# Performance work log

Measured on AMD Instinct MI355X. Metric: run time of the kernel, lower is better.

## Reference

```python
import jax, jax.numpy as jnp
import numpy as np

FP8_MAX = 448.0  # max finite value of float8_e4m3fn
F8 = jnp.float8_e4m3fn


def setup_inputs() -> dict:
    key = jax.random.key(0)
    kx, kw, kb = jax.random.split(key, 3)
    B, S, K, N = 4, 2048, 4096, 16384
    x = jax.random.normal(kx, (B, S, K), dtype=jnp.float32)
    # Pre-quantized symmetric per-tensor FP8 weight: simulate quantization of a
    # realistically initialized fp32 weight with scale ws.
    ws = jnp.float32(0.01)
    w_fp32 = jax.random.normal(kw, (N, K), dtype=jnp.float32) * 0.02
    weight = jnp.clip(w_fp32 / ws, -FP8_MAX, FP8_MAX).astype(F8)  # [N, K] fp8
    weight_scale = jnp.full((1,), ws, dtype=jnp.float32)  # per-tensor strategy
    bias = jax.random.normal(kb, (N,), dtype=jnp.float32) * 0.01
    return {"x": x, "weight": weight, "weight_scale": weight_scale, "bias": bias}


def reference(x, weight, weight_scale, bias):
    # Dynamic per-tensor fp8 quantization of the activation (torchao
    # _input_activation_quant_func_fp8 with PerTensor granularity):
    # (input_scale * weight_scale), plus bias.
    amax = jnp.max(jnp.abs(x))
    x_scale = jnp.maximum(amax, jnp.float32(1e-12)) / FP8_MAX
    xq = jnp.clip(x / x_scale, -FP8_MAX, FP8_MAX).astype(F8).astype(jnp.float32)
    w = weight.astype(jnp.float32)  # [N, K]
    out = jnp.einsum("bsk,nk->bsn", xq, w)  # [B, S, N]
    out = out * (x_scale * weight_scale[0]) + bias
    return out
```

## Files before the change

### kernel.cpp

```cpp
#include <hip/hip_runtime.h>
#include <hip/hip_fp8.h>
#include <hip/hip_fp16.h>
#include <stdint.h>

#define FP8_MAX_V 448.0f

typedef float f32x16 __attribute__((ext_vector_type(16)));
typedef int i32x4 __attribute__((ext_vector_type(4)));
typedef int i32x8 __attribute__((ext_vector_type(8)));

__device__ __forceinline__ uint8_t cvt_fp8(float v) {
    return __hip_cvt_float_to_fp8(fminf(fmaxf(v, -FP8_MAX_V), FP8_MAX_V),
                                  __HIP_SATFINITE, __HIP_E4M3);
}

__global__ void fp8lin_probe(const uint32_t* __restrict__ w, unsigned* __restrict__ flag,
                             unsigned* __restrict__ amax_bits) {
    __shared__ unsigned s32, s16, s4;
    if (threadIdx.x == 0) { s32 = 0u; s16 = 0u; s4 = 0u; *amax_bits = 0u; }
    __syncthreads();
    unsigned o32 = 0u, o16 = 0u, o4 = 0u;
    for (int i = threadIdx.x; i < 4096; i += 256) {
        uint32_t v = w[i];
        o32 |= v & 0x000FFFFFu;
        uint32_t h0 = v & 0xFFFFu, h1 = v >> 16;
        o16 |= (h0 & 0x7Fu) | (h1 & 0x7Fu);
        o4  |= (h0 & 0x0Fu) | (h1 & 0x0Fu);
    }
    atomicOr(&s32, o32); atomicOr(&s16, o16); atomicOr(&s4, o4);
    __syncthreads();
    if (threadIdx.x == 0)
        *flag = (s32 == 0u) ? 0u : (s16 == 0u) ? 1u : (s4 == 0u) ? 2u : 3u;
}

__global__ void fp8lin_amax(const float4* __restrict__ x, unsigned* __restrict__ amax_bits, long n4) {
    float m = 0.f;
    long stride = (long)gridDim.x * blockDim.x;
    for (long i = blockIdx.x * (long)blockDim.x + threadIdx.x; i < n4; i += stride) {
        float4 v = x[i];
        m = fmaxf(m, fmaxf(fmaxf(fabsf(v.x), fabsf(v.y)), fmaxf(fabsf(v.z), fabsf(v.w))));
    }
#pragma unroll
    for (int o = 32; o; o >>= 1) m = fmaxf(m, __shfl_xor(m, o));
    if ((threadIdx.x & 63) == 0) atomicMax(amax_bits, __float_as_uint(m));
}

__global__ void fp8lin_quantpack(const float* __restrict__ x, const unsigned* __restrict__ amax_bits,
                                 uchar4* __restrict__ apack, int M, int K) {
    float s = fmaxf(__uint_as_float(*amax_bits), 1e-12f) / FP8_MAX_V;
    const int NKT = K >> 6;
    const long units = ((long)M * K) >> 2;
    long stride = (long)gridDim.x * blockDim.x;
    for (long u = blockIdx.x * (long)blockDim.x + threadIdx.x; u < units; u += stride) {
        long b2 = u & 7;
        long r = (u >> 3) & 31;
        long q = (u >> 8) & 1;
        long v = u >> 9;
        long row = (v / NKT) * 32 + r;
        long k = (v % NKT) * 64 + q * 32 + b2 * 4;
        float4 t = *(const float4*)(x + row * (long)K + k);
        uchar4 o;
        o.x = cvt_fp8(t.x / s); o.y = cvt_fp8(t.y / s);
        o.z = cvt_fp8(t.z / s); o.w = cvt_fp8(t.w / s);
        apack[u] = o;
    }
}

__global__ void fp8lin_packw(const void* __restrict__ wsrc, const unsigned* __restrict__ flag,
                             uint8_t* __restrict__ pack, int N, int K) {
    const int NKT = K >> 6;
    const long units = ((long)N * K) >> 6;
    unsigned f = *flag;
    long stride = (long)gridDim.x * blockDim.x;
    for (long u = blockIdx.x * (long)blockDim.x + threadIdx.x; u < units; u += stride) {
        int r = (int)(u & 31);
        long v = u >> 5;
        long row = (v / NKT) * 32 + r;
        long kbase = (long)(v % NKT) * 64;
        uint32_t wv[16];
        if (f == 0u) {
            const float4* s = (const float4*)((const float*)wsrc + row * K + kbase);
#pragma unroll
            for (int i = 0; i < 16; ++i) {
                float4 t = s[i];
                wv[i] = (uint32_t)cvt_fp8(t.x) | ((uint32_t)cvt_fp8(t.y) << 8) |
                        ((uint32_t)cvt_fp8(t.z) << 16) | ((uint32_t)cvt_fp8(t.w) << 24);
            }
        } else if (f == 1u) {
            const __half* s = (const __half*)wsrc + row * K + kbase;
#pragma unroll
            for (int i = 0; i < 16; ++i) {
                uint32_t a = 0;
#pragma unroll
                for (int j = 0; j < 4; ++j) a |= (uint32_t)cvt_fp8(__half2float(s[4 * i + j])) << (8 * j);
                wv[i] = a;
            }
        } else if (f == 2u) {
            const uint16_t* s = (const uint16_t*)wsrc + row * K + kbase;
#pragma unroll
            for (int i = 0; i < 16; ++i) {
                uint32_t a = 0;
#pragma unroll
                for (int j = 0; j < 4; ++j)
                    a |= (uint32_t)cvt_fp8(__uint_as_float((uint32_t)s[4 * i + j] << 16)) << (8 * j);
                wv[i] = a;
            }
        } else {
            const uint32_t* s = (const uint32_t*)((const uint8_t*)wsrc + row * K + kbase);
#pragma unroll
            for (int i = 0; i < 16; ++i) wv[i] = s[i];
        }
        uint8_t* d0 = pack + (v * 64 + r) * 32;
        uint8_t* d1 = pack + (v * 64 + 32 + r) * 32;
        i32x4 lo0 = { (int)wv[0], (int)wv[1], (int)wv[2], (int)wv[3] };
        i32x4 lo1 = { (int)wv[4], (int)wv[5], (int)wv[6], (int)wv[7] };
        i32x4 hi0 = { (int)wv[8], (int)wv[9], (int)wv[10], (int)wv[11] };
        i32x4 hi1 = { (int)wv[12], (int)wv[13], (int)wv[14], (int)wv[15] };
        *(i32x4*)(d0) = lo0; *(i32x4*)(d0 + 16) = lo1;
        *(i32x4*)(d1) = hi0; *(i32x4*)(d1 + 16) = hi1;
    }
}

#define BM 256
#define BN 128
#define BK 64

#define LOADF(bv, src, koff) do {                                      \
    const uint8_t* _p = (src) + (koff);                                \
    i32x4 _l0 = *(const i32x4*)(_p);                                   \
    i32x4 _l1 = *(const i32x4*)(_p + 16);                              \
    bv[0] = _l0[0]; bv[1] = _l0[1]; bv[2] = _l0[2]; bv[3] = _l0[3];    \
    bv[4] = _l1[0]; bv[5] = _l1[1]; bv[6] = _l1[2]; bv[7] = _l1[3];    \
} while (0)

#define MFMA_MX(A, B, C) __builtin_amdgcn_mfma_scale_f32_32x32x64_f8f6f4( \
    (A), (B), (C), 0, 0, 0, (int)0x7f7f7f7f, 0, (int)0x7f7f7f7f)

__global__ __launch_bounds__(256, 2) void fp8lin_gemm(
    const uint8_t* __restrict__ Apack,
    const uint8_t* __restrict__ Bpack,
    const unsigned* __restrict__ amax_bits,
    const float* __restrict__ wscale,
    const float* __restrict__ bias,
    float* __restrict__ out,
    int M, int N, int K) {
    const int tid = threadIdx.x;
    const int wid = tid >> 6;
    const int lane = tid & 63;
    const int wm = wid >> 1;
    const int wn = wid & 1;

    const int nbx = gridDim.x;
    const int orig = blockIdx.y * nbx + blockIdx.x;
    const int cpx = (gridDim.x * gridDim.y) >> 3;
    const int swzb = (orig & 7) * cpx + (orig >> 3);
    const int brow = (swzb / nbx) * BM;
    const int bcol = (swzb % nbx) * BN;

    const int NKT = K >> 6;
    const int mt0 = (brow >> 5) + wm * 4;
    const uint8_t* pA0 = Apack + ((size_t)(mt0 + 0) * NKT * 64 + lane) * 32;
    const uint8_t* pA1 = Apack + ((size_t)(mt0 + 1) * NKT * 64 + lane) * 32;
    const uint8_t* pA2 = Apack + ((size_t)(mt0 + 2) * NKT * 64 + lane) * 32;
    const uint8_t* pA3 = Apack + ((size_t)(mt0 + 3) * NKT * 64 + lane) * 32;
    const uint8_t* pB0 = Bpack + ((size_t)((bcol >> 5) + wn * 2) * NKT * 64 + lane) * 32;
    const uint8_t* pB1 = pB0 + (size_t)NKT * 2048;

    f32x16 acc[4][2];
#pragma unroll
    for (int mi = 0; mi < 4; ++mi)
#pragma unroll
        for (int ni = 0; ni < 2; ++ni)
#pragma unroll
            for (int r = 0; r < 16; ++r) acc[mi][ni][r] = 0.0f;

    i32x8 a0, a1, a2, a3, b0, b1;
    LOADF(a0, pA0, 0); LOADF(a1, pA1, 0);
    LOADF(a2, pA2, 0); LOADF(a3, pA3, 0);
    LOADF(b0, pB0, 0); LOADF(b1, pB1, 0);

    const int NT = K / BK;
#pragma unroll 1
    for (int t = 0; t < NT; ++t) {
        __builtin_amdgcn_s_setprio(1);
        acc[0][0] = MFMA_MX(a0, b0, acc[0][0]);
        acc[1][0] = MFMA_MX(a1, b0, acc[1][0]);
        acc[2][0] = MFMA_MX(a2, b0, acc[2][0]);
        acc[3][0] = MFMA_MX(a3, b0, acc[3][0]);
        acc[0][1] = MFMA_MX(a0, b1, acc[0][1]);
        acc[1][1] = MFMA_MX(a1, b1, acc[1][1]);
        acc[2][1] = MFMA_MX(a2, b1, acc[2][1]);
        acc[3][1] = MFMA_MX(a3, b1, acc[3][1]);
        __builtin_amdgcn_s_setprio(0);
        if (t + 1 < NT) {
            size_t off = (size_t)(t + 1) * 2048;
            LOADF(a0, pA0, off); LOADF(a1, pA1, off);
            LOADF(a2, pA2, off); LOADF(a3, pA3, off);
            LOADF(b0, pB0, off); LOADF(b1, pB1, off);
        }
    }

    float s = (fmaxf(__uint_as_float(*amax_bits), 1e-12f) / FP8_MAX_V) * wscale[0];
    const int l31 = lane & 31;
    const int q = lane >> 5;
    const int colg = bcol + wn * 64 + l31;
    const int rowg0 = brow + wm * 128 + 4 * q;
#pragma unroll
    for (int ni = 0; ni < 2; ++ni) {
        int col = colg + ni * 32;
        float bv = bias[col];
#pragma unroll
        for (int mi = 0; mi < 4; ++mi) {
            int rb = rowg0 + mi * 32;
#pragma unroll
            for (int reg = 0; reg < 16; ++reg) {
                int row = rb + (reg & 3) + 8 * (reg >> 2);
                __builtin_nontemporal_store(acc[mi][ni][reg] * s + bv,
                                            out + (size_t)row * N + col);
            }
        }
    }
}

extern "C" void kernel_launch(void* const* d_in, const int* in_sizes, int n_in,
                              void* d_out, int out_size, void* d_ws, size_t ws_size,
                              hipStream_t stream) {
    const float* x = (const float*)d_in[0];
    const void* w = d_in[1];
    const float* wscale = (const float*)d_in[2];
    const float* bias = (const float*)d_in[3];
    float* out = (float*)d_out;

    const int Bb = 4, S = 2048, K = 4096, N = 16384;
    const int M = Bb * S;
    const long nx = (long)M * K;

    unsigned* amax_bits = (unsigned*)d_ws;
    unsigned* wflag = (unsigned*)((char*)d_ws + 32);
    uint8_t* apack = (uint8_t*)((char*)d_ws + 256);
    uint8_t* bpack = (uint8_t*)((char*)d_ws + 256 + nx);

    fp8lin_probe<<<1, 256, 0, stream>>>((const uint32_t*)w, wflag, amax_bits);
    fp8lin_amax<<<2048, 256, 0, stream>>>((const float4*)x, amax_bits, nx / 4);
    fp8lin_quantpack<<<2048, 256, 0, stream>>>(x, amax_bits, (uchar4*)apack, M, K);
    fp8lin_packw<<<2048, 256, 0, stream>>>(w, wflag, bpack, N, K);

    dim3 grid(N / BN, M / BM);
    fp8lin_gemm<<<grid, 256, 0, stream>>>(apack, bpack, amax_bits, wscale, bias, out, M, N, K);
}
```

Baseline: 820.6 us.

## Software-pipeline GEMM loads with split MFMA halves and manual vmcnt waits

```diff
diff --git a/kernel.cpp b/kernel.cpp
--- a/kernel.cpp
+++ b/kernel.cpp
@@ -125,16 +125,33 @@
 #define BN 128
 #define BK 64
 
-#define LOADF(bv, src, koff) do {                                      \
-    const uint8_t* _p = (src) + (koff);                                \
+#define LDU(bv, ub, t) do {                                            \
+    const uint8_t* _p = (ub) + (size_t)(t) * 2048 + voff;              \
     i32x4 _l0 = *(const i32x4*)(_p);                                   \
     i32x4 _l1 = *(const i32x4*)(_p + 16);                              \
     bv[0] = _l0[0]; bv[1] = _l0[1]; bv[2] = _l0[2]; bv[3] = _l0[3];    \
     bv[4] = _l1[0]; bv[5] = _l1[1]; bv[6] = _l1[2]; bv[7] = _l1[3];    \
 } while (0)
 
+#define WAITVM(N) asm volatile("s_waitcnt vmcnt(" #N ")" ::: "memory")
+
 #define MFMA_MX(A, B, C) __builtin_amdgcn_mfma_scale_f32_32x32x64_f8f6f4( \
     (A), (B), (C), 0, 0, 0, (int)0x7f7f7f7f, 0, (int)0x7f7f7f7f)
+
+#define P1(B0, B1) do {                               \
+    __builtin_amdgcn_s_setprio(1);                    \
+    acc[0][0] = MFMA_MX(a0, B0, acc[0][0]);           \
+    acc[1][0] = MFMA_MX(a1, B0, acc[1][0]);           \
+    acc[0][1] = MFMA_MX(a0, B1, acc[0][1]);           \
+    acc[1][1] = MFMA_MX(a1, B1, acc[1][1]);           \
+    __builtin_amdgcn_s_setprio(0); } while (0)
+#define P2(B0, B1) do {                               \
+    __builtin_amdgcn_s_setprio(1);                    \
+    acc[2][0] = MFMA_MX(a2, B0, acc[2][0]);           \
+    acc[3][0] = MFMA_MX(a3, B0, acc[3][0]);           \
+    acc[2][1] = MFMA_MX(a2, B1, acc[2][1]);           \
+    acc[3][1] = MFMA_MX(a3, B1, acc[3][1]);           \
+    __builtin_amdgcn_s_setprio(0); } while (0)
 
 __global__ __launch_bounds__(256, 2) void fp8lin_gemm(
     const uint8_t* __restrict__ Apack,
@@ -158,13 +175,15 @@
     const int bcol = (swzb % nbx) * BN;
 
     const int NKT = K >> 6;
+    const size_t TSTRIDE = (size_t)NKT * 2048;
     const int mt0 = (brow >> 5) + wm * 4;
-    const uint8_t* pA0 = Apack + ((size_t)(mt0 + 0) * NKT * 64 + lane) * 32;
-    const uint8_t* pA1 = Apack + ((size_t)(mt0 + 1) * NKT * 64 + lane) * 32;
-    const uint8_t* pA2 = Apack + ((size_t)(mt0 + 2) * NKT * 64 + lane) * 32;
-    const uint8_t* pA3 = Apack + ((size_t)(mt0 + 3) * NKT * 64 + lane) * 32;
-    const uint8_t* pB0 = Bpack + ((size_t)((bcol >> 5) + wn * 2) * NKT * 64 + lane) * 32;
-    const uint8_t* pB1 = pB0 + (size_t)NKT * 2048;
+    const uint8_t* uA0 = Apack + (size_t)(mt0 + 0) * TSTRIDE;
+    const uint8_t* uA1 = Apack + (size_t)(mt0 + 1) * TSTRIDE;
+    const uint8_t* uA2 = Apack + (size_t)(mt0 + 2) * TSTRIDE;
+    const uint8_t* uA3 = Apack + (size_t)(mt0 + 3) * TSTRIDE;
+    const uint8_t* uB0 = Bpack + (size_t)((bcol >> 5) + wn * 2) * TSTRIDE;
+    const uint8_t* uB1 = uB0 + TSTRIDE;
+    const int voff = lane * 32;
 
     f32x16 acc[4][2];
 #pragma unroll
@@ -174,29 +193,36 @@
 #pragma unroll
             for (int r = 0; r < 16; ++r) acc[mi][ni][r] = 0.0f;
 
-    i32x8 a0, a1, a2, a3, b0, b1;
-    LOADF(a0, pA0, 0); LOADF(a1, pA1, 0);
-    LOADF(a2, pA2, 0); LOADF(a3, pA3, 0);
-    LOADF(b0, pB0, 0); LOADF(b1, pB1, 0);
+    i32x8 a0, a1, a2, a3, bE0, bE1, bO0, bO1;
+
+    LDU(bE0, uB0, 0); LDU(bE1, uB1, 0);
+    LDU(a0, uA0, 0);  LDU(a1, uA1, 0);
+    LDU(a2, uA2, 0);  LDU(a3, uA3, 0);
+    LDU(bO0, uB0, 1); LDU(bO1, uB1, 1);
 
     const int NT = K / BK;
 #pragma unroll 1
-    for (int t = 0; t < NT; ++t) {
-        __builtin_amdgcn_s_setprio(1);
-        acc[0][0] = MFMA_MX(a0, b0, acc[0][0]);
-        acc[1][0] = MFMA_MX(a1, b0, acc[1][0]);
-        acc[2][0] = MFMA_MX(a2, b0, acc[2][0]);
-        acc[3][0] = MFMA_MX(a3, b0, acc[3][0]);
-        acc[0][1] = MFMA_MX(a0, b1, acc[0][1]);
-        acc[1][1] = MFMA_MX(a1, b1, acc[1][1]);
-        acc[2][1] = MFMA_MX(a2, b1, acc[2][1]);
-        acc[3][1] = MFMA_MX(a3, b1, acc[3][1]);
-        __builtin_amdgcn_s_setprio(0);
-        if (t + 1 < NT) {
-            size_t off = (size_t)(t + 1) * 2048;
-            LOADF(a0, pA0, off); LOADF(a1, pA1, off);
-            LOADF(a2, pA2, off); LOADF(a3, pA3, off);
-            LOADF(b0, pB0, off); LOADF(b1, pB1, off);
+    for (int tp = 0; tp < NT; tp += 2) {
+        WAITVM(8);
+        P1(bE0, bE1);
+        LDU(a0, uA0, tp + 1); LDU(a1, uA1, tp + 1);
+        WAITVM(8);
+        P2(bE0, bE1);
+        LDU(a2, uA2, tp + 1); LDU(a3, uA3, tp + 1);
+        if (tp + 2 < NT) {
+            LDU(bE0, uB0, tp + 2); LDU(bE1, uB1, tp + 2);
+            WAITVM(8);
+            P1(bO0, bO1);
+            LDU(a0, uA0, tp + 2); LDU(a1, uA1, tp + 2);
+            WAITVM(8);
+            P2(bO0, bO1);
+            LDU(a2, uA2, tp + 2); LDU(a3, uA3, tp + 2);
+            LDU(bO0, uB0, tp + 3); LDU(bO1, uB1, tp + 3);
+        } else {
+            WAITVM(4);
+            P1(bO0, bO1);
+            WAITVM(0);
+            P2(bO0, bO1);
         }
     }
 
```

Measured after the change: 805.3 us. Within noise of the previous version (-1.9%).
